# Optimization experiments

Measured on AMD Instinct MI355X. Metric: run time of the kernel, lower is better.

## Reference

```python
import jax, jax.numpy as jnp
import numpy as np

D_MODEL = 1024
H = 16
D_K = D_MODEL // H
WINDOW = 256
NEG = -1.0e9


def setup_inputs() -> dict:
    key = jax.random.key(0)
    ks = jax.random.split(key, 12)
    B, S = 1, 4096
    scale = 1.0 / np.sqrt(D_MODEL)
    inp = {
        'q': jax.random.normal(ks[0], (B, S, D_MODEL), dtype=jnp.float32),
        'k': jax.random.normal(ks[1], (B, S, D_MODEL), dtype=jnp.float32),
        'v': jax.random.normal(ks[2], (B, S, D_MODEL), dtype=jnp.float32),
        'w_q': jax.random.normal(ks[3], (D_MODEL, D_MODEL), dtype=jnp.float32) * scale,
        'b_q': jnp.zeros((D_MODEL,), dtype=jnp.float32),
        'w_k': jax.random.normal(ks[4], (D_MODEL, D_MODEL), dtype=jnp.float32) * scale,
        'b_k': jnp.zeros((D_MODEL,), dtype=jnp.float32),
        'w_v': jax.random.normal(ks[5], (D_MODEL, D_MODEL), dtype=jnp.float32) * scale,
        'b_v': jnp.zeros((D_MODEL,), dtype=jnp.float32),
        'w_o': jax.random.normal(ks[6], (D_MODEL, D_MODEL), dtype=jnp.float32) * scale,
        'b_o': jnp.zeros((D_MODEL,), dtype=jnp.float32),
    }
    return inp


def _local_mask(seq_len: int, window_size: int) -> jnp.ndarray:
    left = (window_size - 1) // 2
    right = window_size - 1 - left
    row = jnp.arange(seq_len)[:, None]
    col = jnp.arange(seq_len)[None, :]
    return (col >= row - left) & (col <= row + right)  # [S, S] bool


def reference(q, k, v, w_q, b_q, w_k, b_k, w_v, b_v, w_o, b_o):
    B, Sq, _ = q.shape
    Sk = k.shape[1]
    # projections (torch Linear: x @ W.T + b) -> [B, h, S, d_k]
    query = (q @ w_q.T + b_q).reshape(B, Sq, H, D_K).transpose(0, 2, 1, 3)
    key = (k @ w_k.T + b_k).reshape(B, Sk, H, D_K).transpose(0, 2, 1, 3)
    value = (v @ w_v.T + b_v).reshape(B, Sk, H, D_K).transpose(0, 2, 1, 3)

    scores = jnp.einsum('bhqd,bhkd->bhqk', query, key) / jnp.sqrt(
        jnp.asarray(D_K, dtype=query.dtype))
    if Sq == Sk:
        mask = _local_mask(Sq, WINDOW)  # [S, S]
        scores = jnp.where(mask[None, None], scores, jnp.asarray(NEG, scores.dtype))
    attn = jax.nn.softmax(scores, axis=-1)
    x = jnp.einsum('bhqk,bhkd->bhqd', attn, value)
    x = x.transpose(0, 2, 1, 3).reshape(B, Sq, D_MODEL)
    return x @ w_o.T + b_o
```

## Files before the change

### kernel.cpp

```cpp
#include <hip/hip_runtime.h>

#define SEQ 4096
#define DM 1024
#define NH 16
#define DK 64

typedef _Float16 half8 __attribute__((ext_vector_type(8)));
typedef _Float16 half4v __attribute__((ext_vector_type(4)));
typedef float f32x4 __attribute__((ext_vector_type(4)));

#define MFMA16(a, b, c) __builtin_amdgcn_mfma_f32_16x16x32_f16((a), (b), (c), 0, 0, 0)
#define GLOAD_LDS(g, l)                                                                  \
    __builtin_amdgcn_global_load_lds((const __attribute__((address_space(1))) void*)(g), \
                                     (__attribute__((address_space(3))) void*)(l), 16, 0, 0)

__device__ __forceinline__ float dpp_max16(float x) {
    x = fmaxf(x, __int_as_float(__builtin_amdgcn_update_dpp(
                     0, __float_as_int(x), 0xB1, 0xF, 0xF, true)));
    x = fmaxf(x, __int_as_float(__builtin_amdgcn_update_dpp(
                     0, __float_as_int(x), 0x4E, 0xF, 0xF, true)));
    x = fmaxf(x, __int_as_float(__builtin_amdgcn_update_dpp(
                     0, __float_as_int(x), 0x124, 0xF, 0xF, true)));
    x = fmaxf(x, __int_as_float(__builtin_amdgcn_update_dpp(
                     0, __float_as_int(x), 0x128, 0xF, 0xF, true)));
    return x;
}

__global__ void cvt_all(const float* __restrict__ q, const float* __restrict__ k,
                        const float* __restrict__ v, const float* __restrict__ wq,
                        const float* __restrict__ wk, const float* __restrict__ wv,
                        const float* __restrict__ wo, _Float16* __restrict__ qh,
                        _Float16* __restrict__ kh, _Float16* __restrict__ vh,
                        _Float16* __restrict__ wqh, _Float16* __restrict__ wkh,
                        _Float16* __restrict__ wvh, _Float16* __restrict__ woh) {
    int z = blockIdx.y;
    const float* src;
    _Float16* dst;
    int n;
    switch (z) {
    case 0: src = q;  dst = qh;  n = SEQ * DM; break;
    case 1: src = k;  dst = kh;  n = SEQ * DM; break;
    case 2: src = v;  dst = vh;  n = SEQ * DM; break;
    case 3: src = wq; dst = wqh; n = DM * DM;  break;
    case 4: src = wk; dst = wkh; n = DM * DM;  break;
    case 5: src = wv; dst = wvh; n = DM * DM;  break;
    default: src = wo; dst = woh; n = DM * DM; break;
    }
    int idx = (blockIdx.x * 256 + threadIdx.x) * 8;
    if (idx >= n) return;
    float4 f0 = *(const float4*)(src + idx);
    float4 f1 = *(const float4*)(src + idx + 4);
    half8 h;
    h[0] = (_Float16)f0.x; h[1] = (_Float16)f0.y; h[2] = (_Float16)f0.z; h[3] = (_Float16)f0.w;
    h[4] = (_Float16)f1.x; h[5] = (_Float16)f1.y; h[6] = (_Float16)f1.z; h[7] = (_Float16)f1.w;
    *(half8*)(dst + idx) = h;
}

template <int MT>
__device__ __forceinline__ void gemm_bk64(const _Float16* __restrict__ A,
                                          const _Float16* __restrict__ B, int m0, int n0,
                                          _Float16* As, _Float16* Bs, f32x4 (*acc)[4]) {
    constexpr int MI = MT / 32;
    constexpr int ACH = MT / 64;
    const int tid = threadIdx.x;
    const int wave = tid >> 6, lane = tid & 63;
    const int quad = lane >> 4, l16 = lane & 15;
    const int wr = (wave >> 1) * (MT / 2);
    const int wc = (wave & 1) * 64;
    const int srow = tid >> 2, scol = (tid & 3) * 8;

    for (int k0 = 0; k0 < DM; k0 += 64) {
#pragma unroll
        for (int p = 0; p < 2; ++p) {
            int kc = k0 + p * 32 + scol;
#pragma unroll
            for (int j = 0; j < ACH; ++j)
                GLOAD_LDS(A + (size_t)(m0 + j * 64 + srow) * DM + kc,
                          As + p * (MT * 32) + j * 2048 + tid * 8);
#pragma unroll
            for (int j = 0; j < 2; ++j)
                GLOAD_LDS(B + (size_t)(n0 + j * 64 + srow) * DM + kc,
                          Bs + p * 4096 + j * 2048 + tid * 8);
        }
        __syncthreads();
#pragma unroll
        for (int p = 0; p < 2; ++p) {
            half8 af[MI], bf[4];
#pragma unroll
            for (int mi = 0; mi < MI; ++mi)
                af[mi] = *(const half8*)&As[p * (MT * 32) + (wr + mi * 16 + l16) * 32 + quad * 8];
#pragma unroll
            for (int ni = 0; ni < 4; ++ni)
                bf[ni] = *(const half8*)&Bs[p * 4096 + (wc + ni * 16 + l16) * 32 + quad * 8];
#pragma unroll
            for (int mi = 0; mi < MI; ++mi)
#pragma unroll
                for (int ni = 0; ni < 4; ++ni)
                    acc[mi][ni] = MFMA16(af[mi], bf[ni], acc[mi][ni]);
        }
        __syncthreads();
    }
}

__global__ void __launch_bounds__(256, 3) gemm_qkv(
    const _Float16* __restrict__ qh, const _Float16* __restrict__ kh,
    const _Float16* __restrict__ vh, const _Float16* __restrict__ wqh,
    const _Float16* __restrict__ wkh, const _Float16* __restrict__ wvh,
    const float* __restrict__ bq, const float* __restrict__ bk, const float* __restrict__ bv,
    _Float16* __restrict__ Qo, _Float16* __restrict__ Ko, _Float16* __restrict__ Vt) {
    __shared__ _Float16 As[2 * 128 * 32];
    __shared__ _Float16 Bs[2 * 128 * 32];
    int z = blockIdx.z;
    const _Float16 *A, *B;
    const float* bias;
    float scale;
    if (z == 0) { A = qh; B = wqh; bias = bq; scale = 0.125f; }
    else if (z == 1) { A = kh; B = wkh; bias = bk; scale = 1.0f; }
    else { A = vh; B = wvh; bias = bv; scale = 1.0f; }

    int m0 = blockIdx.x * 128;
    int n0 = blockIdx.y * 128;
    f32x4 acc[4][4] = {};
    gemm_bk64<128>(A, B, m0, n0, As, Bs, acc);

    const int tid = threadIdx.x;
    const int wave = tid >> 6, lane = tid & 63;
    const int quad = lane >> 4, l16 = lane & 15;
    const int wr = (wave >> 1) * 64;
    const int wc = (wave & 1) * 64;
    float bs[4];
#pragma unroll
    for (int ni = 0; ni < 4; ++ni) bs[ni] = bias[n0 + wc + ni * 16 + l16];

    if (z < 2) {
        _Float16* C = (z == 0) ? Qo : Ko;
#pragma unroll
        for (int mi = 0; mi < 4; ++mi)
#pragma unroll
            for (int ni = 0; ni < 4; ++ni) {
                int m = m0 + wr + mi * 16 + quad * 4;
                int n = n0 + wc + ni * 16 + l16;
#pragma unroll
                for (int r = 0; r < 4; ++r)
                    C[(size_t)(m + r) * DM + n] = (_Float16)((acc[mi][ni][r] + bs[ni]) * scale);
            }
    } else {
#pragma unroll
        for (int mi = 0; mi < 4; ++mi)
#pragma unroll
            for (int ni = 0; ni < 4; ++ni) {
                int m = m0 + wr + mi * 16 + quad * 4;
                int n = n0 + wc + ni * 16 + l16;
                half4v p;
#pragma unroll
                for (int r = 0; r < 4; ++r) p[r] = (_Float16)(acc[mi][ni][r] + bs[ni]);
                *(half4v*)(Vt + (size_t)n * SEQ + m) = p;
            }
    }
}

__global__ void __launch_bounds__(256, 3) gemm_out(const _Float16* __restrict__ Xh,
                                                   const _Float16* __restrict__ woh,
                                                   const float* __restrict__ bo,
                                                   float* __restrict__ out) {
    __shared__ _Float16 As[2 * 64 * 32];
    __shared__ _Float16 Bs[2 * 128 * 32];
    int m0 = blockIdx.x * 64;
    int n0 = blockIdx.y * 128;
    f32x4 acc[2][4] = {};
    gemm_bk64<64>(Xh, woh, m0, n0, As, Bs, acc);

    const int tid = threadIdx.x;
    const int wave = tid >> 6, lane = tid & 63;
    const int quad = lane >> 4, l16 = lane & 15;
    const int wr = (wave >> 1) * 32;
    const int wc = (wave & 1) * 64;
#pragma unroll
    for (int mi = 0; mi < 2; ++mi)
#pragma unroll
        for (int ni = 0; ni < 4; ++ni) {
            int m = m0 + wr + mi * 16 + quad * 4;
            int n = n0 + wc + ni * 16 + l16;
            float b = bo[n];
#pragma unroll
            for (int r = 0; r < 4; ++r) out[(size_t)(m + r) * DM + n] = acc[mi][ni][r] + b;
        }
}

__global__ void attn_kernel(const _Float16* __restrict__ Q, const _Float16* __restrict__ K,
                            const _Float16* __restrict__ Vt, _Float16* __restrict__ X) {
    __shared__ _Float16 Pl[4][16][32];
    int tid = threadIdx.x;
    int wave = tid >> 6, lane = tid & 63;
    int quad = lane >> 4, l16 = lane & 15;
    int h = blockIdx.y;
    int bx = ((blockIdx.x & 7) << 3) + (blockIdx.x >> 3);
    int q0 = bx * 64 + wave * 16;

    const _Float16* Qp = Q + (size_t)(q0 + l16) * DM + h * DK + quad * 8;
    half8 aq0 = *(const half8*)(Qp);
    half8 aq1 = *(const half8*)(Qp + 32);
    const half8 ones = {(_Float16)1, (_Float16)1, (_Float16)1, (_Float16)1,
                        (_Float16)1, (_Float16)1, (_Float16)1, (_Float16)1};

    float rowM[4], rowL[4];
    f32x4 o[4] = {};
#pragma unroll
    for (int r = 0; r < 4; ++r) { rowM[r] = -__builtin_inff(); rowL[r] = 0.f; }

    int kstart = (q0 > 127) ? ((q0 - 127) & ~31) : 0;
    int kend = q0 + 143;
    if (kend > SEQ - 1) kend = SEQ - 1;

    for (int kt = kstart; kt <= kend; kt += 32) {
        f32x4 s[2];
#pragma unroll
        for (int cf = 0; cf < 2; ++cf) {
            int krow = kt + cf * 16 + l16;
            const _Float16* Kp = K + (size_t)krow * DM + h * DK + quad * 8;
            half8 b0 = *(const half8*)(Kp);
            half8 b1 = *(const half8*)(Kp + 32);
            f32x4 z = {};
            z = MFMA16(aq0, b0, z);
            z = MFMA16(aq1, b1, z);
            s[cf] = z;
        }
        const bool full = (kt >= q0 - 112) && (kt <= q0 + 97);
        float alpha[4];
#pragma unroll
        for (int r = 0; r < 4; ++r) {
            float x0 = s[0][r], x1 = s[1][r];
            if (!full) {
                int row = q0 + quad * 4 + r;
                int key0 = kt + l16, key1 = kt + 16 + l16;
                if (key0 < row - 127 || key0 > row + 128) x0 = -1e30f;
                if (key1 < row - 127 || key1 > row + 128) x1 = -1e30f;
            }
            float t = dpp_max16(fmaxf(x0, x1));
            float mnew = fmaxf(rowM[r], t);
            alpha[r] = __expf(rowM[r] - mnew);
            float p0 = __expf(x0 - mnew);
            float p1 = __expf(x1 - mnew);
            Pl[wave][quad * 4 + r][l16] = (_Float16)p0;
            Pl[wave][quad * 4 + r][l16 + 16] = (_Float16)p1;
            rowM[r] = mnew;
        }
        half8 ap = *(const half8*)&Pl[wave][l16][quad * 8];
        f32x4 ts = {};
        ts = MFMA16(ap, ones, ts);
#pragma unroll
        for (int r = 0; r < 4; ++r) rowL[r] = rowL[r] * alpha[r] + ts[r];
#pragma unroll
        for (int ni = 0; ni < 4; ++ni) {
#pragma unroll
            for (int r = 0; r < 4; ++r) o[ni][r] *= alpha[r];
            const _Float16* Vp = Vt + (size_t)(h * DK + ni * 16 + l16) * SEQ + kt + quad * 8;
            half8 bv = *(const half8*)(Vp);
            o[ni] = MFMA16(ap, bv, o[ni]);
        }
    }

    float rinv[4];
#pragma unroll
    for (int r = 0; r < 4; ++r) rinv[r] = 1.0f / rowL[r];
#pragma unroll
    for (int ni = 0; ni < 4; ++ni) {
        int n = h * DK + ni * 16 + l16;
#pragma unroll
        for (int r = 0; r < 4; ++r) {
            int m = q0 + quad * 4 + r;
            X[(size_t)m * DM + n] = (_Float16)(o[ni][r] * rinv[r]);
        }
    }
}

extern "C" void kernel_launch(void* const* d_in, const int* in_sizes, int n_in, void* d_out,
                              int out_size, void* d_ws, size_t ws_size, hipStream_t stream) {
    const float* q  = (const float*)d_in[0];
    const float* k  = (const float*)d_in[1];
    const float* v  = (const float*)d_in[2];
    const float* wq = (const float*)d_in[3];
    const float* bq = (const float*)d_in[4];
    const float* wk = (const float*)d_in[5];
    const float* bk = (const float*)d_in[6];
    const float* wv = (const float*)d_in[7];
    const float* bv = (const float*)d_in[8];
    const float* wo = (const float*)d_in[9];
    const float* bo = (const float*)d_in[10];

    const size_t SZ_T = (size_t)SEQ * DM * sizeof(_Float16);
    const size_t SZ_W = (size_t)DM * DM * sizeof(_Float16);
    char* p = (char*)d_ws;
    _Float16* qh  = (_Float16*)(p);
    _Float16* kh  = (_Float16*)(p + SZ_T);
    _Float16* vh  = (_Float16*)(p + 2 * SZ_T);
    _Float16* wqh = (_Float16*)(p + 3 * SZ_T);
    _Float16* wkh = (_Float16*)(p + 3 * SZ_T + SZ_W);
    _Float16* wvh = (_Float16*)(p + 3 * SZ_T + 2 * SZ_W);
    _Float16* woh = (_Float16*)(p + 3 * SZ_T + 3 * SZ_W);
    _Float16* Qo  = (_Float16*)(p + 3 * SZ_T + 4 * SZ_W);
    _Float16* Ko  = (_Float16*)(p + 4 * SZ_T + 4 * SZ_W);
    _Float16* Vt  = (_Float16*)(p + 5 * SZ_T + 4 * SZ_W);
    _Float16* Xh  = qh;

    cvt_all<<<dim3(2048, 7), 256, 0, stream>>>(q, k, v, wq, wk, wv, wo, qh, kh, vh, wqh, wkh,
                                               wvh, woh);
    gemm_qkv<<<dim3(32, 8, 3), 256, 0, stream>>>(qh, kh, vh, wqh, wkh, wvh, bq, bk, bv, Qo, Ko,
                                                 Vt);
    attn_kernel<<<dim3(SEQ / 64, NH), 256, 0, stream>>>(Qo, Ko, Vt, Xh);
    gemm_out<<<dim3(64, 8), 256, 0, stream>>>(Xh, woh, bo, (float*)d_out);
}
```

Measured before the change: 205.6 us.

## Split attention key range across two wave groups and merge partial softmax

The attention kernel now launches 512 threads per block. Each 16-row query tile is handled by two waves, and each wave processes half of the local-window key tiles. The second wave writes its partial output, running max and running sum to shared memory. The first wave then merges them with the usual online-softmax rescaling. This aims to shorten the serial key loop per wave and expose more parallelism, at the cost of a block barrier, extra shared memory and some duplicated query loads.

Measured after the change: 239.8 us. 1.17x slower.

```diff
diff --git a/kernel.cpp b/kernel.cpp
--- a/kernel.cpp
+++ b/kernel.cpp
@@ -187,15 +187,19 @@
         }
 }
 
-__global__ void attn_kernel(const _Float16* __restrict__ Q, const _Float16* __restrict__ K,
-                            const _Float16* __restrict__ Vt, _Float16* __restrict__ X) {
-    __shared__ _Float16 Pl[4][16][32];
+__global__ void __launch_bounds__(512, 8) attn_kernel(const _Float16* __restrict__ Q,
+                                                      const _Float16* __restrict__ K,
+                                                      const _Float16* __restrict__ Vt,
+                                                      _Float16* __restrict__ X) {
+    __shared__ _Float16 Pl[8][16][32];
+    __shared__ float mbuf[4][24][64];
     int tid = threadIdx.x;
     int wave = tid >> 6, lane = tid & 63;
     int quad = lane >> 4, l16 = lane & 15;
+    int qw = wave & 3, half = wave >> 2;
     int h = blockIdx.y;
     int bx = ((blockIdx.x & 7) << 3) + (blockIdx.x >> 3);
-    int q0 = bx * 64 + wave * 16;
+    int q0 = bx * 64 + qw * 16;
 
     const _Float16* Qp = Q + (size_t)(q0 + l16) * DM + h * DK + quad * 8;
     half8 aq0 = *(const half8*)(Qp);
@@ -211,8 +215,12 @@
     int kstart = (q0 > 127) ? ((q0 - 127) & ~31) : 0;
     int kend = q0 + 143;
     if (kend > SEQ - 1) kend = SEQ - 1;
-
-    for (int kt = kstart; kt <= kend; kt += 32) {
+    int nt = ((kend - kstart) >> 5) + 1;
+    int nh = (nt + 1) >> 1;
+    int kbeg = half ? (kstart + nh * 32) : kstart;
+    int klast = half ? (kstart + (nt - 1) * 32) : (kstart + (nh - 1) * 32);
+
+    for (int kt = kbeg; kt <= klast; kt += 32) {
         f32x4 s[2];
 #pragma unroll
         for (int cf = 0; cf < 2; ++cf) {
@@ -260,16 +268,38 @@
         }
     }
 
-    float rinv[4];
-#pragma unroll
-    for (int r = 0; r < 4; ++r) rinv[r] = 1.0f / rowL[r];
-#pragma unroll
-    for (int ni = 0; ni < 4; ++ni) {
-        int n = h * DK + ni * 16 + l16;
+    if (half) {
+#pragma unroll
+        for (int ni = 0; ni < 4; ++ni)
+#pragma unroll
+            for (int r = 0; r < 4; ++r) mbuf[qw][ni * 4 + r][lane] = o[ni][r];
 #pragma unroll
         for (int r = 0; r < 4; ++r) {
-            int m = q0 + quad * 4 + r;
-            X[(size_t)m * DM + n] = (_Float16)(o[ni][r] * rinv[r]);
+            mbuf[qw][16 + r][lane] = rowM[r];
+            mbuf[qw][20 + r][lane] = rowL[r];
+        }
+    }
+    __syncthreads();
+    if (!half) {
+        float a0[4], a1[4], rinv[4];
+#pragma unroll
+        for (int r = 0; r < 4; ++r) {
+            float m1 = mbuf[qw][16 + r][lane];
+            float l1 = mbuf[qw][20 + r][lane];
+            float M = fmaxf(rowM[r], m1);
+            a0[r] = __expf(rowM[r] - M);
+            a1[r] = __expf(m1 - M);
+            rinv[r] = 1.0f / (rowL[r] * a0[r] + l1 * a1[r]);
+        }
+#pragma unroll
+        for (int ni = 0; ni < 4; ++ni) {
+            int n = h * DK + ni * 16 + l16;
+#pragma unroll
+            for (int r = 0; r < 4; ++r) {
+                int m = q0 + quad * 4 + r;
+                float oc = o[ni][r] * a0[r] + mbuf[qw][ni * 4 + r][lane] * a1[r];
+                X[(size_t)m * DM + n] = (_Float16)(oc * rinv[r]);
+            }
         }
     }
 }
@@ -307,6 +337,6 @@
                                                wvh, woh);
     gemm_qkv<<<dim3(32, 8, 3), 256, 0, stream>>>(qh, kh, vh, wqh, wkh, wvh, bq, bk, bv, Qo, Ko,
                                                  Vt);
-    attn_kernel<<<dim3(SEQ / 64, NH), 256, 0, stream>>>(Qo, Ko, Vt, Xh);
+    attn_kernel<<<dim3(SEQ / 64, NH), 512, 0, stream>>>(Qo, Ko, Vt, Xh);
     gemm_out<<<dim3(64, 8), 256, 0, stream>>>(Xh, woh, bo, (float*)d_out);
 }
```

## Prefetch K/V tiles and use lazy softmax rescaling in local attention kernel

Applied to the files above, without the earlier changes.

The attention loop now loads the next K tile into registers while computing the current one, and issues the V loads at the top of each iteration so their latency overlaps the QK^T MFMAs and the softmax. The online-softmax max update is made lazy: the running max and accumulators are rescaled only when some row's new max exceeds the stored one by more than a threshold, which skips most per-iteration exp and multiply work. Launch bounds are added to steer register allocation. The changes raise register pressure, and the fp16 P values can grow up to e^8 before a rescale, which trades some precision headroom for less work.

Measured after the change: 205.0 us. About the same (-0.3%).

```diff
diff --git a/kernel.cpp b/kernel.cpp
--- a/kernel.cpp
+++ b/kernel.cpp
@@ -187,8 +187,10 @@
         }
 }
 
-__global__ void attn_kernel(const _Float16* __restrict__ Q, const _Float16* __restrict__ K,
-                            const _Float16* __restrict__ Vt, _Float16* __restrict__ X) {
+__global__ void __launch_bounds__(256, 4) attn_kernel(const _Float16* __restrict__ Q,
+                                                      const _Float16* __restrict__ K,
+                                                      const _Float16* __restrict__ Vt,
+                                                      _Float16* __restrict__ X) {
     __shared__ _Float16 Pl[4][16][32];
     int tid = threadIdx.x;
     int wave = tid >> 6, lane = tid & 63;
@@ -203,6 +205,9 @@
     const half8 ones = {(_Float16)1, (_Float16)1, (_Float16)1, (_Float16)1,
                         (_Float16)1, (_Float16)1, (_Float16)1, (_Float16)1};
 
+    const _Float16* Kbase = K + h * DK + quad * 8;
+    const _Float16* Vbase = Vt + (size_t)(h * DK + l16) * SEQ + quad * 8;
+
     float rowM[4], rowL[4];
     f32x4 o[4] = {};
 #pragma unroll
@@ -212,21 +217,40 @@
     int kend = q0 + 143;
     if (kend > SEQ - 1) kend = SEQ - 1;
 
+    half8 ka[4];
+#pragma unroll
+    for (int cf = 0; cf < 2; ++cf) {
+        const _Float16* Kp = Kbase + (size_t)(kstart + cf * 16 + l16) * DM;
+        ka[cf * 2] = *(const half8*)Kp;
+        ka[cf * 2 + 1] = *(const half8*)(Kp + 32);
+    }
+
     for (int kt = kstart; kt <= kend; kt += 32) {
+        half8 vb[4];
+#pragma unroll
+        for (int ni = 0; ni < 4; ++ni)
+            vb[ni] = *(const half8*)(Vbase + (size_t)(ni * 16) * SEQ + kt);
+
         f32x4 s[2];
 #pragma unroll
         for (int cf = 0; cf < 2; ++cf) {
-            int krow = kt + cf * 16 + l16;
-            const _Float16* Kp = K + (size_t)krow * DM + h * DK + quad * 8;
-            half8 b0 = *(const half8*)(Kp);
-            half8 b1 = *(const half8*)(Kp + 32);
             f32x4 z = {};
-            z = MFMA16(aq0, b0, z);
-            z = MFMA16(aq1, b1, z);
+            z = MFMA16(aq0, ka[cf * 2], z);
+            z = MFMA16(aq1, ka[cf * 2 + 1], z);
             s[cf] = z;
         }
+
+        if (kt + 32 <= kend) {
+#pragma unroll
+            for (int cf = 0; cf < 2; ++cf) {
+                const _Float16* Kp = Kbase + (size_t)(kt + 32 + cf * 16 + l16) * DM;
+                ka[cf * 2] = *(const half8*)Kp;
+                ka[cf * 2 + 1] = *(const half8*)(Kp + 32);
+            }
+        }
+
         const bool full = (kt >= q0 - 112) && (kt <= q0 + 97);
-        float alpha[4];
+        float t[4], g = -3e38f;
 #pragma unroll
         for (int r = 0; r < 4; ++r) {
             float x0 = s[0][r], x1 = s[1][r];
@@ -235,29 +259,38 @@
                 int key0 = kt + l16, key1 = kt + 16 + l16;
                 if (key0 < row - 127 || key0 > row + 128) x0 = -1e30f;
                 if (key1 < row - 127 || key1 > row + 128) x1 = -1e30f;
-            }
-            float t = dpp_max16(fmaxf(x0, x1));
-            float mnew = fmaxf(rowM[r], t);
-            alpha[r] = __expf(rowM[r] - mnew);
-            float p0 = __expf(x0 - mnew);
-            float p1 = __expf(x1 - mnew);
+                s[0][r] = x0; s[1][r] = x1;
+            }
+            t[r] = dpp_max16(fmaxf(x0, x1));
+            g = fmaxf(g, t[r] - rowM[r]);
+        }
+
+        if (__any(g > 8.0f)) {
+#pragma unroll
+            for (int r = 0; r < 4; ++r) {
+                float mnew = fmaxf(rowM[r], t[r]);
+                float a = __expf(rowM[r] - mnew);
+                rowM[r] = mnew;
+                rowL[r] *= a;
+#pragma unroll
+                for (int ni = 0; ni < 4; ++ni) o[ni][r] *= a;
+            }
+        }
+
+#pragma unroll
+        for (int r = 0; r < 4; ++r) {
+            float p0 = __expf(s[0][r] - rowM[r]);
+            float p1 = __expf(s[1][r] - rowM[r]);
             Pl[wave][quad * 4 + r][l16] = (_Float16)p0;
             Pl[wave][quad * 4 + r][l16 + 16] = (_Float16)p1;
-            rowM[r] = mnew;
         }
         half8 ap = *(const half8*)&Pl[wave][l16][quad * 8];
         f32x4 ts = {};
         ts = MFMA16(ap, ones, ts);
 #pragma unroll
-        for (int r = 0; r < 4; ++r) rowL[r] = rowL[r] * alpha[r] + ts[r];
-#pragma unroll
-        for (int ni = 0; ni < 4; ++ni) {
-#pragma unroll
-            for (int r = 0; r < 4; ++r) o[ni][r] *= alpha[r];
-            const _Float16* Vp = Vt + (size_t)(h * DK + ni * 16 + l16) * SEQ + kt + quad * 8;
-            half8 bv = *(const half8*)(Vp);
-            o[ni] = MFMA16(ap, bv, o[ni]);
-        }
+        for (int r = 0; r < 4; ++r) rowL[r] += ts[r];
+#pragma unroll
+        for (int ni = 0; ni < 4; ++ni) o[ni] = MFMA16(ap, vb[ni], o[ni]);
     }
 
     float rinv[4];
```

## Stage block-shared K window in swizzled LDS and prefetch V per tile

Applied to the files above, without the earlier changes.

The attention kernel now loads the 320-row K window covering all four waves of a block into LDS once, using async global-to-LDS loads with an XOR swizzle. Previously each wave read K from global memory on its own, so overlapping windows were fetched repeatedly. V fragments are loaded at the top of each key tile so their latency overlaps the QK MFMA and softmax work. The P staging buffer gets padded rows and the kernel gets launch bounds; the larger LDS footprint and extra registers may limit occupancy.

Result: faster. 193.4 us (-5.9%).

```diff
diff --git a/kernel.cpp b/kernel.cpp
--- a/kernel.cpp
+++ b/kernel.cpp
@@ -187,15 +187,30 @@
         }
 }
 
-__global__ void attn_kernel(const _Float16* __restrict__ Q, const _Float16* __restrict__ K,
-                            const _Float16* __restrict__ Vt, _Float16* __restrict__ X) {
-    __shared__ _Float16 Pl[4][16][32];
+__global__ void __launch_bounds__(256, 4) attn_kernel(const _Float16* __restrict__ Q,
+                                                      const _Float16* __restrict__ K,
+                                                      const _Float16* __restrict__ Vt,
+                                                      _Float16* __restrict__ X) {
+    __shared__ _Float16 Ks[320 * 64];
+    __shared__ _Float16 Pl[4][16][40];
     int tid = threadIdx.x;
     int wave = tid >> 6, lane = tid & 63;
     int quad = lane >> 4, l16 = lane & 15;
     int h = blockIdx.y;
     int bx = ((blockIdx.x & 7) << 3) + (blockIdx.x >> 3);
-    int q0 = bx * 64 + wave * 16;
+    int q0b = bx * 64;
+    int q0 = q0b + wave * 16;
+    int kspan0 = q0b - 128;
+
+    const _Float16* Kg = K + h * DK;
+#pragma unroll
+    for (int i = 0; i < 10; ++i) {
+        int U = i * 256 + tid;
+        int row = U >> 3, u = U & 7;
+        int rg = kspan0 + row;
+        rg = rg < 0 ? 0 : (rg > SEQ - 1 ? SEQ - 1 : rg);
+        GLOAD_LDS(Kg + (size_t)rg * DM + ((u ^ (row & 7)) << 3), Ks + U * 8);
+    }
 
     const _Float16* Qp = Q + (size_t)(q0 + l16) * DM + h * DK + quad * 8;
     half8 aq0 = *(const half8*)(Qp);
@@ -211,15 +226,23 @@
     int kstart = (q0 > 127) ? ((q0 - 127) & ~31) : 0;
     int kend = q0 + 143;
     if (kend > SEQ - 1) kend = SEQ - 1;
+    const int xk = l16 & 7;
+
+    __syncthreads();
 
     for (int kt = kstart; kt <= kend; kt += 32) {
+        int rel = kt - kspan0;
+        half8 vb[4];
+#pragma unroll
+        for (int ni = 0; ni < 4; ++ni)
+            vb[ni] = *(const half8*)(Vt + (size_t)(h * DK + ni * 16 + l16) * SEQ + kt + quad * 8);
+
         f32x4 s[2];
 #pragma unroll
         for (int cf = 0; cf < 2; ++cf) {
-            int krow = kt + cf * 16 + l16;
-            const _Float16* Kp = K + (size_t)krow * DM + h * DK + quad * 8;
-            half8 b0 = *(const half8*)(Kp);
-            half8 b1 = *(const half8*)(Kp + 32);
+            int rr = rel + cf * 16 + l16;
+            half8 b0 = *(const half8*)&Ks[rr * 64 + ((quad ^ xk) << 3)];
+            half8 b1 = *(const half8*)&Ks[rr * 64 + (((quad + 4) ^ xk) << 3)];
             f32x4 z = {};
             z = MFMA16(aq0, b0, z);
             z = MFMA16(aq1, b1, z);
@@ -254,9 +277,7 @@
         for (int ni = 0; ni < 4; ++ni) {
 #pragma unroll
             for (int r = 0; r < 4; ++r) o[ni][r] *= alpha[r];
-            const _Float16* Vp = Vt + (size_t)(h * DK + ni * 16 + l16) * SEQ + kt + quad * 8;
-            half8 bv = *(const half8*)(Vp);
-            o[ni] = MFMA16(ap, bv, o[ni]);
+            o[ni] = MFMA16(ap, vb[ni], o[ni]);
         }
     }
 
```
